# Kernel optimization log

Measured on AMD Instinct MI355X. Metric: run time of the kernel, lower is better.

Reference implementation:

```python
import jax, jax.numpy as jnp
import numpy as np

PRECISION = 2.0 ** 24  # ctx._precision stand-in; factor = sqrt(precision)
SF_CONST = 48.0


def setup_inputs() -> dict:
    key = jax.random.key(0)
    k1, k2, k3 = jax.random.split(key, 3)
    x = jax.random.normal(k1, (16, 128, 128, 128), dtype=jnp.float32)  # NCHW
    W = jax.random.normal(k2, (256, 128, 3, 3), dtype=jnp.float32) * 0.05  # OIHW
    b = jax.random.normal(k3, (256,), dtype=jnp.float32) * 0.1
    return {"x": x, "W": W, "b": b}


def reference(x, W, b):
    # --- quantize() (standard, non-mixture path) ---
    N = float(np.prod(W.shape[1:]))           # in_ch * kh * kw = 1152
    factor = np.sqrt(PRECISION)               # sqrt(ctx._precision)
    sf = np.sqrt(SF_CONST / N)
    w_sum = jnp.sum(jnp.abs(W), axis=(1, 2, 3))          # [O]
    w_sum = jnp.where(w_sum == 0, 1.0, w_sum)
    fw = (factor / sf - np.sqrt(N / 12.0) * 5.0) / w_sum  # [O]
    Wq = jnp.round(W * fw[:, None, None, None])

    # --- forward int-quantized conv ---
    x_max = jnp.max(jnp.abs(x))
    fx = jnp.where(x_max > 0, (factor * sf - 0.5) / x_max, 1.0)
    xq = jnp.round(fx * x)
    y = jax.lax.conv_general_dilated(
        xq, Wq,
        window_strides=(1, 1),
        padding=((1, 1), (1, 1)),
        dimension_numbers=("NCHW", "OIHW", "NCHW"),
    )
    # dequantize per output channel, then fused float bias add
    y = y / (fx * fw[:, None, None]) + b[:, None, None]
    # Activation (ReLU); BN disabled, dropout disabled in this config
    return jax.nn.relu(y)
```

## Files before the change

kernel.cpp:

```cpp
#include <hip/hip_runtime.h>
#include <math.h>


#define FW_NUM 20017.23017802413f
#define FX_NUM 835.5924988699913f
#define WQA_OFF 2048
#define WQB_OFF (640 * 1024)
#define XQ_OFF  (2 * 1024 * 1024)
#define XQ_BYTES 67108864ull

#define CK  16
#define CKP 24
#define JW  130

typedef _Float16 half8 __attribute__((ext_vector_type(8)));
typedef _Float16 half4 __attribute__((ext_vector_type(4)));
typedef float floatx16 __attribute__((ext_vector_type(16)));

__device__ __forceinline__ void gl_lds16(const void* g, void* s) {
    __builtin_amdgcn_global_load_lds((const __attribute__((address_space(1))) void*)g,
                                     (__attribute__((address_space(3))) void*)s, 16, 0, 0);
}

__global__ void xmax_kernel(const float* __restrict__ x, unsigned int* wsu, int n4) {
    int tid = blockIdx.x * blockDim.x + threadIdx.x;
    int stride = gridDim.x * blockDim.x;
    const float4* x4 = (const float4*)x;
    float m = 0.f;
    for (int i = tid; i < n4; i += stride) {
        float4 v = x4[i];
        m = fmaxf(m, fmaxf(fmaxf(fabsf(v.x), fabsf(v.y)), fmaxf(fabsf(v.z), fabsf(v.w))));
    }
    #pragma unroll
    for (int off = 32; off >= 1; off >>= 1)
        m = fmaxf(m, __shfl_down(m, off, 64));
    __shared__ float sm[4];
    if ((threadIdx.x & 63) == 0) sm[threadIdx.x >> 6] = m;
    __syncthreads();
    if (threadIdx.x == 0) {
        m = fmaxf(fmaxf(sm[0], sm[1]), fmaxf(sm[2], sm[3]));
        atomicMax(wsu, __float_as_uint(m));
    }
}

__global__ void wq_kernel(const float* __restrict__ W, float* wsf, int big) {
    int o = blockIdx.x;
    int t = threadIdx.x;
    const float* wrow = W + o * 1152;
    float wv[9];
    float s = 0.f;
    #pragma unroll
    for (int k = 0; k < 9; k++) { wv[k] = wrow[t * 9 + k]; s += fabsf(wv[k]); }
    #pragma unroll
    for (int off = 32; off >= 1; off >>= 1) s += __shfl_down(s, off, 64);
    __shared__ float sred[2];
    __shared__ float sfw;
    if ((t & 63) == 0) sred[t >> 6] = s;
    __syncthreads();
    if (t == 0) {
        float wsum = sred[0] + sred[1];
        if (wsum == 0.f) wsum = 1.f;
        float fw = FW_NUM / wsum;
        wsf[64 + o] = fw;
        sfw = fw;
    }
    __syncthreads();
    float fw = sfw;
    _Float16* wqa = (_Float16*)((char*)wsf + WQA_OFF);
    _Float16* wqb = (_Float16*)((char*)wsf + WQB_OFF);
    int oswz = (o & ~3) | ((o & 3) ^ ((o >> 3) & 3));
    int qflip = (o >> 2) & 1;
    #pragma unroll
    for (int k = 0; k < 9; k++) {
        _Float16 hv = (_Float16)rintf(wv[k] * fw);
        wqa[(o * 9 + k) * 128 + t] = hv;
        if (big) {
            int q = (t >> 3) & 1;
            int qswz = q ^ qflip;
            wqb[(((t >> 4) * 9 + k) * 256 + oswz) * 16 + qswz * 8 + (t & 7)] = hv;
        }
    }
}

__global__ void quantx_kernel(const float* __restrict__ x, const float* __restrict__ wsf,
                              _Float16* __restrict__ xq) {
    int bid = blockIdx.x;
    int h  = bid & 127;
    int cc = (bid >> 7) & 7;
    int n  = bid >> 10;
    float xmax = __uint_as_float(((const unsigned int*)wsf)[0]);
    float fx = xmax > 0.f ? FX_NUM / xmax : 1.0f;
    int w = threadIdx.x;
    const float* xp = x + ((size_t)(n * 128 + cc * 16) * 128 + h) * 128 + w;
    half8 v0, v1;
    #pragma unroll
    for (int ci = 0; ci < 8; ci++)  v0[ci] = (_Float16)rintf(fx * xp[(size_t)ci * 16384]);
    #pragma unroll
    for (int ci = 8; ci < 16; ci++) v1[ci - 8] = (_Float16)rintf(fx * xp[(size_t)ci * 16384]);
    _Float16* op = xq + ((size_t)bid * 128 + w) * 16;
    *(half8*)op = v0;
    *(half8*)(op + 8) = v1;
}

__global__ __launch_bounds__(256, 2) void conv_main(const _Float16* __restrict__ xq,
                                                    const float* __restrict__ bias,
                                                    const float* __restrict__ wsf,
                                                    float* __restrict__ out) {
    __shared__ __align__(16) _Float16 xs[2][18 * 34 * 16];
    __shared__ __align__(16) _Float16 wl[2][9 * 64 * 16];
    __shared__ float sc[64], bz[64];

    float xmax = __uint_as_float(((const unsigned int*)wsf)[0]);
    float fx = xmax > 0.f ? FX_NUM / xmax : 1.0f;

    int bx0 = blockIdx.x;
    int bx = (bx0 & 7) * 256 + (bx0 >> 3);
    int o0 = (bx & 3) << 6;
    int w0 = ((bx >> 2) & 3) << 5;
    int h0 = ((bx >> 4) & 7) << 4;
    int n  = bx >> 7;

    int tid = threadIdx.x;
    int lane = tid & 63;
    int wv = tid >> 6;
    int m32 = lane & 31;
    int q2 = lane >> 5;

    const char* wqb = (const char*)wsf + WQB_OFF;

    int xcol[3];
    #pragma unroll
    for (int kw = 0; kw < 3; ++kw) {
        int j = m32 + kw;
        xcol[kw] = (j * 32 + q2 * 16) ^ ((((j) >> 2) & 7) << 4);
    }
    int wcol = (m32 * 32 + q2 * 16) ^ (((m32 >> 2) & 7) << 4);

    int xsrcoff;
    {
        int jp = 1 + (lane >> 1), qp = lane & 1;
        int t = (jp >> 3) & 3;
        int j = (jp & ~3) | ((jp & 3) ^ t);
        int q = qp ^ ((jp >> 2) & 1);
        xsrcoff = (j - 1) * 32 + q * 16;
    }

    {
        uint4 z = {0u, 0u, 0u, 0u};
        uint4* p = (uint4*)xs;
        for (int i = tid; i < (int)(sizeof(xs) / 16); i += 256) p[i] = z;
        if (tid < 64) {
            float fwv = wsf[64 + o0 + tid];
            sc[tid] = 1.0f / (fx * fwv);
            bz[tid] = bias[o0 + tid];
        }
    }
    __syncthreads();

    floatx16 acc[2][4];
    #pragma unroll
    for (int a1 = 0; a1 < 2; a1++)
        #pragma unroll
        for (int a2 = 0; a2 < 4; a2++)
            #pragma unroll
            for (int e = 0; e < 16; e++) acc[a1][a2][e] = 0.f;

    auto stage_async = [&](int ccs, int tb) {
        for (int s = wv; s < 36; s += 4) {
            if (s < 18) {
                int r = s;
                int h = h0 + r - 1;
                if (h >= 0 && h < 128) {
                    size_t pix = ((size_t)((n * 8 + ccs) * 128 + h)) * 128 + w0;
                    const char* src = (const char*)xq + pix * 32 + xsrcoff;
                    char* dst = (char*)&xs[tb][(r * 34 + 1) * 16];
                    gl_lds16(src, dst);
                }
            } else {
                int t2 = s - 18, tap = t2 >> 1, g = t2 & 1;
                const char* src = wqb + ((size_t)(ccs * 9 + tap) * 256 + o0) * 32 + g * 1024 + (size_t)lane * 16;
                char* dst = (char*)&wl[tb][tap * 64 * 16] + g * 1024;
                gl_lds16(src, dst);
            }
        }
    };
    auto halo_load = [&](int ccs) -> half8 {
        half8 v = {};
        if (tid < 72) {
            int r = tid >> 2, sd = (tid >> 1) & 1, g = tid & 1;
            int h = h0 + r - 1;
            int wh = sd ? (w0 + 32) : (w0 - 1);
            if (h >= 0 && h < 128 && wh >= 0 && wh < 128)
                v = *(const half8*)(xq + (((size_t)((n * 8 + ccs) * 128 + h)) * 128 + wh) * 16 + g * 8);
        }
        return v;
    };
    auto halo_store = [&](int tb, half8 v) {
        if (tid < 72) {
            int r = tid >> 2, sd = (tid >> 1) & 1, g = tid & 1;
            int h = h0 + r - 1;
            int wh = sd ? (w0 + 32) : (w0 - 1);
            if (h >= 0 && h < 128 && wh >= 0 && wh < 128)
                *(half8*)((char*)&xs[tb][0] + r * 1088 + (sd ? 33 * 32 : 0) + g * 16) = v;
        }
    };

    {
        half8 hv = halo_load(0);
        stage_async(0, 0);
        halo_store(0, hv);
    }
    __syncthreads();

    for (int cc = 0; cc < 8; ++cc) {
        int cb = cc & 1;
        half8 hn = {};
        if (cc < 7) {
            hn = halo_load(cc + 1);
            stage_async(cc + 1, cb ^ 1);
        }

        const char* xb = (const char*)&xs[cb][0] + wv * (4 * 1088);
        const char* wb = (const char*)&wl[cb][0];
        #pragma unroll
        for (int kw = 0; kw < 3; ++kw) {
            half8 xf[6];
            #pragma unroll
            for (int srow = 0; srow < 6; ++srow)
                xf[srow] = *(const half8*)(xb + srow * 1088 + xcol[kw]);
            #pragma unroll
            for (int kh = 0; kh < 3; ++kh) {
                const char* wp = wb + (kh * 3 + kw) * 2048 + wcol;
                half8 wf0 = *(const half8*)wp;
                half8 wf1 = *(const half8*)(wp + 1024);
                #pragma unroll
                for (int p = 0; p < 4; ++p) {
                    acc[0][p] = __builtin_amdgcn_mfma_f32_32x32x16_f16(wf0, xf[p + kh], acc[0][p], 0, 0, 0);
                    acc[1][p] = __builtin_amdgcn_mfma_f32_32x32x16_f16(wf1, xf[p + kh], acc[1][p], 0, 0, 0);
                }
            }
        }

        if (cc < 7) halo_store(cb ^ 1, hn);
        __syncthreads();
    }

    #pragma unroll
    for (int ot = 0; ot < 2; ++ot) {
        #pragma unroll
        for (int e = 0; e < 16; ++e) {
            int o_loc = ot * 32 + (e & 3) + 8 * (e >> 2) + 4 * q2;
            float scale = sc[o_loc];
            float bv = bz[o_loc];
            #pragma unroll
            for (int p = 0; p < 4; ++p) {
                int h = h0 + wv * 4 + p;
                float v = fmaxf(fmaf(acc[ot][p][e], scale, bv), 0.f);
                out[(((size_t)(n * 256 + o0 + o_loc)) * 128 + h) * 128 + w0 + m32] = v;
            }
        }
    }
}

__global__ __launch_bounds__(256, 2) void conv_fallback(const float* __restrict__ x,
                                                        const float* __restrict__ bias,
                                                        const float* __restrict__ wsf,
                                                        float* __restrict__ out) {
    __shared__ __align__(16) _Float16 xs[6 * JW * CKP];
    __shared__ __align__(16) _Float16 wlds[9 * 64 * CKP];

    const unsigned int* wsu = (const unsigned int*)wsf;
    float xmax = __uint_as_float(wsu[0]);
    float fx = xmax > 0.f ? FX_NUM / xmax : 1.0f;

    int bx = blockIdx.x;
    int n  = bx >> 5;
    int h0 = (bx & 31) << 2;
    int o0 = blockIdx.y << 6;

    int tid  = threadIdx.x;
    int lane = tid & 63;
    int wave = tid >> 6;
    int m32  = lane & 31;
    int q2   = lane >> 5;

    const _Float16* wq16 = (const _Float16*)((const char*)wsf + WQA_OFF);
    const float* xn = x + (size_t)n * (128 * 128 * 128);

    floatx16 acc[4][2];
    #pragma unroll
    for (int mt = 0; mt < 4; mt++)
        #pragma unroll
        for (int nt = 0; nt < 2; nt++)
            #pragma unroll
            for (int e = 0; e < 16; e++) acc[mt][nt][e] = 0.f;

    if (tid < 192) {
        int r = tid >> 5;
        int s = tid & 31;
        int c = s & 15;
        int j = (s >> 4) ? (JW - 1) : 0;
        xs[(r * JW + j) * CKP + c] = (_Float16)0.f;
    }

    for (int c0 = 0; c0 < 128; c0 += CK) {
        __syncthreads();
        #pragma unroll
        for (int it = 0; it < 12; ++it) {
            int idx = tid + it * 256;
            int j  = (idx & 127) + 1;
            int c4 = (idx >> 7) & 3;
            int r  = idx >> 9;
            int h  = h0 + r - 1;
            float v0 = 0.f, v1 = 0.f, v2 = 0.f, v3 = 0.f;
            if (h >= 0 && h < 128) {
                const float* xp = xn + (size_t)(c0 + c4 * 4) * 16384 + h * 128 + (j - 1);
                v0 = xp[0]; v1 = xp[16384]; v2 = xp[32768]; v3 = xp[49152];
            }
            half4 hv;
            hv[0] = (_Float16)rintf(fx * v0);
            hv[1] = (_Float16)rintf(fx * v1);
            hv[2] = (_Float16)rintf(fx * v2);
            hv[3] = (_Float16)rintf(fx * v3);
            *(half4*)&xs[(r * JW + j) * CKP + c4 * 4] = hv;
        }
        #pragma unroll
        for (int it = 0; it < 5; ++it) {
            int idx = tid + it * 256;
            if (idx < 1152) {
                int o   = idx / 18;
                int rem = idx - o * 18;
                int tap = rem >> 1;
                int g   = rem & 1;
                half8 v = *(const half8*)(wq16 + ((size_t)(o0 + o) * 9 + tap) * 128 + c0 + g * 8);
                *(half8*)&wlds[(tap * 64 + o) * CKP + g * 8] = v;
            }
        }
        __syncthreads();

        const _Float16* xbase = &xs[(wave * JW + m32) * CKP + q2 * 8];
        const _Float16* wbase = &wlds[m32 * CKP + q2 * 8];
        #pragma unroll
        for (int kh = 0; kh < 3; ++kh) {
            #pragma unroll
            for (int kw = 0; kw < 3; ++kw) {
                int tap = kh * 3 + kw;
                half8 b0 = *(const half8*)(wbase + (tap * 64 +  0) * CKP);
                half8 b1 = *(const half8*)(wbase + (tap * 64 + 32) * CKP);
                #pragma unroll
                for (int mt = 0; mt < 4; ++mt) {
                    half8 a = *(const half8*)(xbase + (kh * JW + kw + mt * 32) * CKP);
                    acc[mt][0] = __builtin_amdgcn_mfma_f32_32x32x16_f16(a, b0, acc[mt][0], 0, 0, 0);
                    acc[mt][1] = __builtin_amdgcn_mfma_f32_32x32x16_f16(a, b1, acc[mt][1], 0, 0, 0);
                }
            }
        }
    }

    int h = h0 + wave;
    #pragma unroll
    for (int nt = 0; nt < 2; ++nt) {
        int o = o0 + nt * 32 + m32;
        float fwv = wsf[64 + o];
        float scale = 1.0f / (fx * fwv);
        float bv = bias[o];
        float* op = out + (((size_t)n * 256 + o) * 128 + h) * 128;
        #pragma unroll
        for (int mt = 0; mt < 4; ++mt) {
            #pragma unroll
            for (int g = 0; g < 4; ++g) {
                int w = mt * 32 + 8 * g + 4 * q2;
                float4 r;
                r.x = fmaxf(fmaf(acc[mt][nt][4 * g + 0], scale, bv), 0.f);
                r.y = fmaxf(fmaf(acc[mt][nt][4 * g + 1], scale, bv), 0.f);
                r.z = fmaxf(fmaf(acc[mt][nt][4 * g + 2], scale, bv), 0.f);
                r.w = fmaxf(fmaf(acc[mt][nt][4 * g + 3], scale, bv), 0.f);
                *(float4*)(op + w) = r;
            }
        }
    }
}

extern "C" void kernel_launch(void* const* d_in, const int* in_sizes, int n_in,
                              void* d_out, int out_size, void* d_ws, size_t ws_size,
                              hipStream_t stream) {
    const float* x = (const float*)d_in[0];
    const float* W = (const float*)d_in[1];
    const float* b = (const float*)d_in[2];
    float* out = (float*)d_out;
    float* wsf = (float*)d_ws;

    int big = (ws_size >= (size_t)XQ_OFF + XQ_BYTES) ? 1 : 0;

    hipMemsetAsync(d_ws, 0, 256, stream);

    xmax_kernel<<<1024, 256, 0, stream>>>(x, (unsigned int*)d_ws, (16 * 128 * 128 * 128) / 4);
    wq_kernel<<<256, 128, 0, stream>>>(W, wsf, big);

    if (big) {
        _Float16* xq = (_Float16*)((char*)d_ws + XQ_OFF);
        quantx_kernel<<<16 * 8 * 128, 128, 0, stream>>>(x, wsf, xq);
        conv_main<<<2048, 256, 0, stream>>>(xq, b, wsf, out);
    } else {
        dim3 grid(512, 4);
        conv_fallback<<<grid, 256, 0, stream>>>(x, b, wsf, out);
    }
}
```

Baseline: 501.0 us.

## Unify conv staging into uniform async LDS loads with zero-page halo and waitcnt pipelining

Replaces the split async-stage plus register halo load/store path with a single precomputed set of per-thread global-to-LDS async copies. Padding and out-of-range pixels read from a zeroed scratch page in the workspace, and offsets advance by a stride each channel chunk. The per-iteration syncthreads is replaced by raw barriers with explicit vmcnt waits so the next chunk's loads stay in flight during compute, and s_setprio is raised around the MFMA groups. The change removes halo register traffic and LDS zero-init, but it adds an extra memset and more LDS-slot bookkeeping.

```diff
diff --git a/kernel.cpp b/kernel.cpp
--- a/kernel.cpp
+++ b/kernel.cpp
@@ -6,6 +6,7 @@
 #define FX_NUM 835.5924988699913f
 #define WQA_OFF 2048
 #define WQB_OFF (640 * 1024)
+#define ZP_OFF  (1536 * 1024)
 #define XQ_OFF  (2 * 1024 * 1024)
 #define XQ_BYTES 67108864ull
 
@@ -106,8 +107,8 @@
                                                     const float* __restrict__ bias,
                                                     const float* __restrict__ wsf,
                                                     float* __restrict__ out) {
-    __shared__ __align__(16) _Float16 xs[2][18 * 34 * 16];
-    __shared__ __align__(16) _Float16 wl[2][9 * 64 * 16];
+    __shared__ __align__(16) _Float16 xs[2][10240];
+    __shared__ __align__(16) _Float16 wl[2][9728];
     __shared__ float sc[64], bz[64];
 
     float xmax = __uint_as_float(((const unsigned int*)wsf)[0]);
@@ -126,7 +127,7 @@
     int m32 = lane & 31;
     int q2 = lane >> 5;
 
-    const char* wqb = (const char*)wsf + WQB_OFF;
+    const char* wsb = (const char*)wsf;
 
     int xcol[3];
     #pragma unroll
@@ -136,24 +137,56 @@
     }
     int wcol = (m32 * 32 + q2 * 16) ^ (((m32 >> 2) & 7) << 4);
 
-    int xsrcoff;
-    {
-        int jp = 1 + (lane >> 1), qp = lane & 1;
-        int t = (jp >> 3) & 3;
-        int j = (jp & ~3) | ((jp & 3) ^ t);
-        int q = qp ^ ((jp >> 2) & 1);
-        xsrcoff = (j - 1) * 32 + q * 16;
-    }
-
-    {
-        uint4 z = {0u, 0u, 0u, 0u};
-        uint4* p = (uint4*)xs;
-        for (int i = tid; i < (int)(sizeof(xs) / 16); i += 256) p[i] = z;
-        if (tid < 64) {
-            float fwv = wsf[64 + o0 + tid];
-            sc[tid] = 1.0f / (fx * fwv);
-            bz[tid] = bias[o0 + tid];
-        }
+    int goff[10];
+    int gstr[10];
+    #pragma unroll
+    for (int k = 0; k < 10; ++k) {
+        int s = wv + 4 * k;
+        int off, str;
+        if (s < 20) {
+            int slot = s * 64 + lane;
+            int r = (slot * 241) >> 14;
+            int spi = slot - r * 68;
+            int u = spi ^ ((spi >> 3) & 7);
+            int j = u >> 1, q = u & 1;
+            int h = h0 + r - 1, w = w0 + j - 1;
+            bool ok = (slot < 1224) && (h >= 0) && (h < 128) && (w >= 0) && (w < 128);
+            if (ok) {
+                off = XQ_OFF + n * 4194304 + (h * 128 + w) * 32 + q * 16;
+                str = 524288;
+            } else {
+                off = ZP_OFF + lane * 16;
+                str = 0;
+            }
+        } else if (s < 38) {
+            int t2 = s - 20, tap = t2 >> 1, g = t2 & 1;
+            off = WQB_OFF + (tap * 256 + o0) * 32 + g * 1024 + lane * 16;
+            str = 73728;
+        } else {
+            off = ZP_OFF + lane * 16;
+            str = 0;
+        }
+        goff[k] = off;
+        gstr[k] = str;
+    }
+
+    auto stage = [&](int tb) {
+        #pragma unroll
+        for (int k = 0; k < 10; ++k) {
+            int s = wv + 4 * k;
+            char* dst;
+            if (s < 20)      dst = (char*)&xs[tb][0] + s * 1024;
+            else if (s < 38) dst = (char*)&wl[tb][0] + (s - 20) * 1024;
+            else             dst = (char*)&wl[tb][0] + 18 * 1024;
+            gl_lds16(wsb + goff[k], dst);
+            goff[k] += gstr[k];
+        }
+    };
+
+    if (tid < 64) {
+        float fwv = wsf[64 + o0 + tid];
+        sc[tid] = 1.0f / (fx * fwv);
+        bz[tid] = bias[o0 + tid];
     }
     __syncthreads();
 
@@ -165,60 +198,18 @@
             #pragma unroll
             for (int e = 0; e < 16; e++) acc[a1][a2][e] = 0.f;
 
-    auto stage_async = [&](int ccs, int tb) {
-        for (int s = wv; s < 36; s += 4) {
-            if (s < 18) {
-                int r = s;
-                int h = h0 + r - 1;
-                if (h >= 0 && h < 128) {
-                    size_t pix = ((size_t)((n * 8 + ccs) * 128 + h)) * 128 + w0;
-                    const char* src = (const char*)xq + pix * 32 + xsrcoff;
-                    char* dst = (char*)&xs[tb][(r * 34 + 1) * 16];
-                    gl_lds16(src, dst);
-                }
-            } else {
-                int t2 = s - 18, tap = t2 >> 1, g = t2 & 1;
-                const char* src = wqb + ((size_t)(ccs * 9 + tap) * 256 + o0) * 32 + g * 1024 + (size_t)lane * 16;
-                char* dst = (char*)&wl[tb][tap * 64 * 16] + g * 1024;
-                gl_lds16(src, dst);
-            }
-        }
-    };
-    auto halo_load = [&](int ccs) -> half8 {
-        half8 v = {};
-        if (tid < 72) {
-            int r = tid >> 2, sd = (tid >> 1) & 1, g = tid & 1;
-            int h = h0 + r - 1;
-            int wh = sd ? (w0 + 32) : (w0 - 1);
-            if (h >= 0 && h < 128 && wh >= 0 && wh < 128)
-                v = *(const half8*)(xq + (((size_t)((n * 8 + ccs) * 128 + h)) * 128 + wh) * 16 + g * 8);
-        }
-        return v;
-    };
-    auto halo_store = [&](int tb, half8 v) {
-        if (tid < 72) {
-            int r = tid >> 2, sd = (tid >> 1) & 1, g = tid & 1;
-            int h = h0 + r - 1;
-            int wh = sd ? (w0 + 32) : (w0 - 1);
-            if (h >= 0 && h < 128 && wh >= 0 && wh < 128)
-                *(half8*)((char*)&xs[tb][0] + r * 1088 + (sd ? 33 * 32 : 0) + g * 16) = v;
-        }
-    };
-
-    {
-        half8 hv = halo_load(0);
-        stage_async(0, 0);
-        halo_store(0, hv);
-    }
-    __syncthreads();
+    stage(0);
 
     for (int cc = 0; cc < 8; ++cc) {
         int cb = cc & 1;
-        half8 hn = {};
+        __builtin_amdgcn_s_barrier();
         if (cc < 7) {
-            hn = halo_load(cc + 1);
-            stage_async(cc + 1, cb ^ 1);
-        }
+            stage(cb ^ 1);
+            asm volatile("s_waitcnt vmcnt(10)" ::: "memory");
+        } else {
+            asm volatile("s_waitcnt vmcnt(0)" ::: "memory");
+        }
+        __builtin_amdgcn_s_barrier();
 
         const char* xb = (const char*)&xs[cb][0] + wv * (4 * 1088);
         const char* wb = (const char*)&wl[cb][0];
@@ -233,16 +224,15 @@
                 const char* wp = wb + (kh * 3 + kw) * 2048 + wcol;
                 half8 wf0 = *(const half8*)wp;
                 half8 wf1 = *(const half8*)(wp + 1024);
+                __builtin_amdgcn_s_setprio(1);
                 #pragma unroll
                 for (int p = 0; p < 4; ++p) {
                     acc[0][p] = __builtin_amdgcn_mfma_f32_32x32x16_f16(wf0, xf[p + kh], acc[0][p], 0, 0, 0);
                     acc[1][p] = __builtin_amdgcn_mfma_f32_32x32x16_f16(wf1, xf[p + kh], acc[1][p], 0, 0, 0);
                 }
-            }
-        }
-
-        if (cc < 7) halo_store(cb ^ 1, hn);
-        __syncthreads();
+                __builtin_amdgcn_s_setprio(0);
+            }
+        }
     }
 
     #pragma unroll
@@ -393,6 +383,8 @@
     int big = (ws_size >= (size_t)XQ_OFF + XQ_BYTES) ? 1 : 0;
 
     hipMemsetAsync(d_ws, 0, 256, stream);
+    if (big)
+        hipMemsetAsync((char*)d_ws + ZP_OFF, 0, 2048, stream);
 
     xmax_kernel<<<1024, 256, 0, stream>>>(x, (unsigned int*)d_ws, (16 * 128 * 128 * 128) / 4);
     wq_kernel<<<256, 128, 0, stream>>>(W, wsf, big);
```

Result: no change. 497.5 us (-0.7%).
